# Kernel tuning notes

Measured on AMD Instinct MI355X. Metric: run time of the kernel, lower is better.

## Reference

```python
import jax, jax.numpy as jnp
import numpy as np
from jax import lax

# fixed body-part graph: column j lists source nodes i with adj[i,j]!=0
PART_LIST_LIST = [[1], [0, 2, 3, 4], [1], [1], [1, 5], [4]]
HID = 10
IN_DIM = 256


def conv1x1(x, W):  # x:[B,C,H,W], W:[O,C]
    return jnp.einsum('bchw,oc->bohw', x, W)


def bn(x, s, t):  # eval-mode BN folded to per-channel affine
    return x * s[None, :, None, None] + t[None, :, None, None]


def relation(x, W1, s1, t1, W2, s2, t2):
    h = jax.nn.relu(bn(conv1x1(x, W1), s1, t1))
    return jax.nn.relu(bn(conv1x1(h, W2), s2, t2))


def conv3x3(x, W, b):
    y = lax.conv_general_dilated(x, W, (1, 1), 'SAME',
                                 dimension_numbers=('NCHW', 'OIHW', 'NCHW'))
    return y + b[None, :, None, None]


def gru_step(msg, h, Wg, bg, Wc, bc):
    # one ConvGRU step: gates from cat([input, h]), candidate from cat([input, r*h])
    gates = jax.nn.sigmoid(conv3x3(jnp.concatenate([msg, h], axis=1), Wg, bg))
    r, u = jnp.split(gates, 2, axis=1)
    cand = jnp.tanh(conv3x3(jnp.concatenate([msg, r * h], axis=1), Wc, bc))
    return (1.0 - u) * h + u * cand


def _forward(f_node, h_nodes, p_nodes, xp,
             W_dau, b_dau, W_dal, b_dal,
             W_dec1, dec1_s, dec1_t, W_dec2, dec2_s, dec2_t,
             W_att0, W_att1, W_att2, W_att3, W_att4, W_att5, b_att,
             W_proj, proj_s, proj_t, Wg, bg, Wc, bc):
    # decomposition attention maps (Decomp_att): 1x1 conv with bias
    decomp_map_u = conv1x1(h_nodes[0], W_dau) + b_dau[None, :, None, None]  # [B,5,H,W]
    decomp_map_l = conv1x1(h_nodes[1], W_dal) + b_dal[None, :, None, None]  # [B,3,H,W]
    att_u = jax.nn.softmax(decomp_map_u, axis=1)
    att_l = jax.nn.softmax(decomp_map_l, axis=1)

    # Decomposition: relation(cat([parent*att_{i+1}, child_i])), shared weights
    def decomp(parent, child, a):
        return relation(jnp.concatenate([parent * a, child], axis=1),
                        W_dec1, dec1_s, dec1_t, W_dec2, dec2_s, dec2_t)

    dec_u = [decomp(h_nodes[0], p_nodes[i], att_u[:, i + 1:i + 2]) for i in range(4)]
    dec_l = [decomp(h_nodes[1], p_nodes[4 + i], att_l[:, i + 1:i + 2]) for i in range(2)]
    decomp_msgs = jnp.stack(dec_u + dec_l)  # [6,B,10,H,W]

    # Contexture: per-node attention over concatenated neighbor features
    W_atts = [W_att0, W_att1, W_att2, W_att3, W_att4, W_att5]
    atts = []
    for i, plist in enumerate(PART_LIST_LIST):
        ctx = jnp.concatenate([p_nodes[j] for j in plist], axis=1)
        atts.append(jax.nn.sigmoid(conv1x1(ctx, W_atts[i]) + b_att[i]))
    Fdep_att = jnp.stack(atts)  # [6,B,1,H,W]

    modulated = xp[None] * (2.0 - Fdep_att)                     # [6,B,256,H,W]
    proj = jnp.einsum('nbchw,noc->nbohw', modulated, W_proj)    # [6,B,10,H,W]
    proj = jax.nn.relu(proj * proj_s[:, None, :, None, None]
                       + proj_t[:, None, :, None, None])

    message = decomp_msgs + proj
    # per-node ConvGRU update (hidden state = p_node)
    xp_new = jax.vmap(gru_step)(message, p_nodes, Wg, bg, Wc, bc)  # [6,B,10,H,W]
    return xp_new, decomp_map_u, decomp_map_l, Fdep_att


def setup_inputs() -> dict:
    key = jax.random.key(0)
    ks = jax.random.split(key, 32)
    B, H, W = 4, 128, 128
    hd, cd = HID, IN_DIM

    def rn(k, shape, s=0.05):
        return jax.random.normal(k, shape, jnp.float32) * s

    inp = {}
    inp['f_node'] = rn(ks[0], (B, hd, H, W), 1.0)
    inp['h_nodes'] = rn(ks[1], (2, B, hd, H, W), 1.0)
    inp['p_nodes'] = rn(ks[2], (6, B, hd, H, W), 1.0)
    inp['xp'] = rn(ks[3], (B, cd, H, W), 1.0)
    inp['W_dau'] = rn(ks[4], (5, hd));  inp['b_dau'] = rn(ks[5], (5,))
    inp['W_dal'] = rn(ks[6], (3, hd));  inp['b_dal'] = rn(ks[7], (3,))
    inp['W_dec1'] = rn(ks[8], (2 * hd, 2 * hd))
    inp['dec1_s'] = 1.0 + rn(ks[9], (2 * hd,)); inp['dec1_t'] = rn(ks[10], (2 * hd,))
    inp['W_dec2'] = rn(ks[11], (hd, 2 * hd))
    inp['dec2_s'] = 1.0 + rn(ks[12], (hd,));    inp['dec2_t'] = rn(ks[13], (hd,))
    lens = [len(p) for p in PART_LIST_LIST]  # [1,4,1,1,2,1]
    for i in range(6):
        inp[f'W_att{i}'] = rn(ks[14 + i], (1, hd * lens[i]))
    inp['b_att'] = rn(ks[20], (6,))
    inp['W_proj'] = rn(ks[21], (6, hd, cd))
    inp['proj_s'] = 1.0 + rn(ks[22], (6, hd)); inp['proj_t'] = rn(ks[23], (6, hd))
    inp['Wg'] = rn(ks[24], (6, 2 * hd, 2 * hd, 3, 3)); inp['bg'] = rn(ks[25], (6, 2 * hd))
    inp['Wc'] = rn(ks[26], (6, hd, 2 * hd, 3, 3));     inp['bc'] = rn(ks[27], (6, hd))
    return inp


def reference(f_node, h_nodes, p_nodes, xp,
              W_dau, b_dau, W_dal, b_dal,
              W_dec1, dec1_s, dec1_t, W_dec2, dec2_s, dec2_t,
              W_att0, W_att1, W_att2, W_att3, W_att4, W_att5, b_att,
              W_proj, proj_s, proj_t, Wg, bg, Wc, bc):
    return _forward(f_node, h_nodes, p_nodes, xp,
                    W_dau, b_dau, W_dal, b_dal,
                    W_dec1, dec1_s, dec1_t, W_dec2, dec2_s, dec2_t,
                    W_att0, W_att1, W_att2, W_att3, W_att4, W_att5, b_att,
                    W_proj, proj_s, proj_t, Wg, bg, Wc, bc)
```

## Files before the change

### kernel.cpp

```cpp
#include <hip/hip_runtime.h>
#include <math.h>

#define HW    16384
#define WID   128
#define NB    4
#define OFF_U 3932160
#define OFF_L 4259840
#define OFF_F 4456448

#define TCH   24
#define TROW  132
#define T6_N  (6*TROW*TCH)
#define WG_ELEMS   (9*32*TCH)
#define WC_ELEMS   (9*16*TCH)

typedef __attribute__((ext_vector_type(8))) short  short8_t;
typedef __attribute__((ext_vector_type(4))) float  float4_t;

__device__ __forceinline__ float sig_(float x)  { return 1.f/(1.f+__expf(-x)); }
__device__ __forceinline__ float tanh_(float x) { float e=__expf(2.f*x); return 1.f - 2.f/(e+1.f); }
__device__ __forceinline__ unsigned pk2bf(float a, float b){
  unsigned r;
  asm("v_cvt_pk_bf16_f32 %0, %1, %2" : "=v"(r) : "v"(a), "v"(b));
  return r;
}
__device__ __forceinline__ float bf2f(unsigned short s){
  return __uint_as_float(((unsigned)s) << 16);
}
__device__ __forceinline__ int swz1536(int bi){ return (bi & 7)*192 + (bi >> 3); }
__device__ __forceinline__ int swz768 (int bi){ return (bi & 7)*96  + (bi >> 3); }

__global__ __launch_bounds__(256)
void k_att_dec(const float* __restrict__ hn, const float* __restrict__ pnn,
               const float* __restrict__ Wdau, const float* __restrict__ bdau,
               const float* __restrict__ Wdal, const float* __restrict__ bdal,
               const float* __restrict__ Wd1, const float* __restrict__ s1v, const float* __restrict__ t1v,
               const float* __restrict__ Wd2, const float* __restrict__ s2v, const float* __restrict__ t2v,
               const float* __restrict__ Wa0, const float* __restrict__ Wa1, const float* __restrict__ Wa2,
               const float* __restrict__ Wa3, const float* __restrict__ Wa4, const float* __restrict__ Wa5,
               const float* __restrict__ batt,
               float* __restrict__ out, unsigned* __restrict__ wmsg_p)
{
  const int bi  = swz1536(blockIdx.x);
  const int n   = bi >> 8;
  const int g   = (bi & 255)*256 + threadIdx.x;
  const int b   = g >> 14;
  const int pix = g & 16383;

  float h[10];
  float a;
  if (n < 4){
#pragma unroll
    for (int c=0;c<10;c++) h[c] = hn[(b*10+c)*HW + pix];
    float v[5]; float mx = -1e30f;
#pragma unroll
    for (int o=0;o<5;o++){
      float t = bdau[o];
#pragma unroll
      for (int c=0;c<10;c++) t += Wdau[o*10+c]*h[c];
      if (n==0) out[OFF_U + (b*5+o)*HW + pix] = t;
      v[o]=t; mx = fmaxf(mx,t);
    }
    float s=0.f;
#pragma unroll
    for (int o=0;o<5;o++){ v[o]=__expf(v[o]-mx); s+=v[o]; }
    a = v[n+1]/s;
  } else {
#pragma unroll
    for (int c=0;c<10;c++) h[c] = hn[((NB+b)*10+c)*HW + pix];
    float v[3]; float mx = -1e30f;
#pragma unroll
    for (int o=0;o<3;o++){
      float t = bdal[o];
#pragma unroll
      for (int c=0;c<10;c++) t += Wdal[o*10+c]*h[c];
      if (n==4) out[OFF_L + (b*3+o)*HW + pix] = t;
      v[o]=t; mx = fmaxf(mx,t);
    }
    float s=0.f;
#pragma unroll
    for (int o=0;o<3;o++){ v[o]=__expf(v[o]-mx); s+=v[o]; }
    a = v[n-3]/s;
  }

  float child[10];
#pragma unroll
  for (int c=0;c<10;c++) child[c] = pnn[((n*NB+b)*10+c)*HW + pix];

  float af = batt[n];
  if (n==0){
#pragma unroll
    for (int c=0;c<10;c++) af += Wa0[c]*pnn[((1*NB+b)*10+c)*HW+pix];
  } else if (n==1){
#pragma unroll
    for (int c=0;c<10;c++){
      af += Wa1[c]   *pnn[((0*NB+b)*10+c)*HW+pix];
      af += Wa1[10+c]*pnn[((2*NB+b)*10+c)*HW+pix];
      af += Wa1[20+c]*pnn[((3*NB+b)*10+c)*HW+pix];
      af += Wa1[30+c]*pnn[((4*NB+b)*10+c)*HW+pix];
    }
  } else if (n==2){
#pragma unroll
    for (int c=0;c<10;c++) af += Wa2[c]*pnn[((1*NB+b)*10+c)*HW+pix];
  } else if (n==3){
#pragma unroll
    for (int c=0;c<10;c++) af += Wa3[c]*pnn[((1*NB+b)*10+c)*HW+pix];
  } else if (n==4){
#pragma unroll
    for (int c=0;c<10;c++){
      af += Wa4[c]   *pnn[((1*NB+b)*10+c)*HW+pix];
      af += Wa4[10+c]*pnn[((5*NB+b)*10+c)*HW+pix];
    }
  } else {
#pragma unroll
    for (int c=0;c<10;c++) af += Wa5[c]*pnn[((4*NB+b)*10+c)*HW+pix];
  }
  out[OFF_F + (n*NB+b)*HW + pix] = sig_(af);

  float x20[20];
#pragma unroll
  for (int c=0;c<10;c++){ x20[c]=h[c]*a; x20[10+c]=child[c]; }
  float h20[20];
#pragma unroll
  for (int o=0;o<20;o++){
    float acc=0.f;
#pragma unroll
    for (int c=0;c<20;c++) acc += Wd1[o*20+c]*x20[c];
    h20[o] = fmaxf(acc*s1v[o]+t1v[o], 0.f);
  }
  float msg10[10];
#pragma unroll
  for (int o=0;o<10;o++){
    float acc=0.f;
#pragma unroll
    for (int c=0;c<20;c++) acc += Wd2[o*20+c]*h20[c];
    msg10[o] = fmaxf(acc*s2v[o]+t2v[o], 0.f);
  }
#pragma unroll
  for (int p=0;p<5;p++)
    wmsg_p[((size_t)((n*NB+b)*5 + p))*HW + pix] = pk2bf(msg10[2*p], msg10[2*p+1]);
}

__global__ __launch_bounds__(256, 2)
void k_proj(const float* __restrict__ xp, const float* __restrict__ Wp,
            const float* __restrict__ ps, const float* __restrict__ pt,
            const float* __restrict__ outf, unsigned* __restrict__ wmsg_p)
{
  __shared__ __align__(16) unsigned short wlds[64*264];
  const int tid = threadIdx.x;

#pragma unroll
  for (int it=0; it<16; ++it){
    const int e = tid + it*256;
    const int row = e >> 6, q = e & 63;
    uint2 pk; pk.x = 0u; pk.y = 0u;
    if (row < 60){
      const float s = ps[row];
      float4 wv = *reinterpret_cast<const float4*>(Wp + row*256 + q*4);
      pk.x = pk2bf(wv.x*s, wv.y*s);
      pk.y = pk2bf(wv.z*s, wv.w*s);
    }
    *reinterpret_cast<uint2*>(&wlds[row*264 + q*4]) = pk;
  }
  __syncthreads();

  const int l  = tid & 63;
  const int w  = tid >> 6;
  const int lr = l & 15;
  const int lk = l >> 4;

  const int tile = blockIdx.x*4 + w;
  const int P    = tile*16;
  const int b    = P >> 14;
  const int pixb = P & 16383;
  const int px   = pixb + lr;

  const float* xb = xp + (size_t)(b*256)*HW + px;
  float v[64];
#pragma unroll
  for (int ks=0; ks<8; ++ks)
#pragma unroll
    for (int j=0; j<8; ++j)
      v[ks*8+j] = xb[(size_t)(ks*32 + lk*8 + j)*HW];

  short8_t bf[8];
#pragma unroll
  for (int ks=0; ks<8; ++ks){
    union { short8_t s; unsigned u[4]; } bu;
#pragma unroll
    for (int jp=0; jp<4; ++jp)
      bu.u[jp] = pk2bf(v[ks*8+2*jp], v[ks*8+2*jp+1]);
    bf[ks] = bu.s;
  }

  float4_t acc[4];
#pragma unroll
  for (int nf=0;nf<4;nf++){ acc[nf][0]=0.f; acc[nf][1]=0.f; acc[nf][2]=0.f; acc[nf][3]=0.f; }

#pragma unroll
  for (int ks=0; ks<8; ++ks){
#pragma unroll
    for (int nf=0; nf<4; ++nf){
      short8_t wa = *reinterpret_cast<const short8_t*>(&wlds[(nf*16+lr)*264 + ks*32 + lk*8]);
      acc[nf] = __builtin_amdgcn_mfma_f32_16x16x32_bf16(wa, bf[ks], acc[nf], 0,0,0);
    }
  }

#pragma unroll
  for (int nf=0;nf<4;nf++){
#pragma unroll
    for (int jp=0;jp<2;jp++){
      const int row0 = nf*16 + lk*4 + 2*jp;
      if (row0 < 60){
        const unsigned nn = (unsigned)row0 / 10u;
        const int o = row0 - (int)nn*10;
        float att = outf[OFF_F + (nn*NB+b)*HW + pixb + lr];
        float f   = 2.f - att;
        float v0 = fmaxf(f*acc[nf][2*jp]   + pt[row0],   0.f);
        float v1 = fmaxf(f*acc[nf][2*jp+1] + pt[row0+1], 0.f);
        size_t idx = ((size_t)((nn*NB+b)*5 + (o>>1)))*HW + pixb + lr;
        unsigned old = wmsg_p[idx];
        float d0 = bf2f((unsigned short)(old & 0xffffu)) + v0;
        float d1 = bf2f((unsigned short)(old >> 16))     + v1;
        wmsg_p[idx] = pk2bf(d0, d1);
      }
    }
  }
}

__global__ __launch_bounds__(256, 3)
void k_gru_gates(const float* __restrict__ pnn, const float* __restrict__ Wg,
                 const float* __restrict__ bg,
                 const unsigned* __restrict__ wmsg_p, unsigned* __restrict__ wrh_p,
                 unsigned* __restrict__ wu_p)
{
  __shared__ __align__(16) unsigned short tl[T6_N];
  __shared__ __align__(16) unsigned short wl[WG_ELEMS];
  const int bi = swz768(blockIdx.x);
  const int n  = bi >> 7;
  const int b  = (bi >> 5) & 3;
  const int y0 = (bi & 31) * 4;
  const int tid = threadIdx.x;

  const int base_nb  = (n*NB+b)*10;
  const int base_nb5 = (n*NB+b)*5;
  const float* pb = pnn + (size_t)base_nb*HW;

  short8_t zz = {0,0,0,0,0,0,0,0};
#pragma unroll
  for (int it=0; it<10; ++it){
    const int e = tid*8 + it*2048;
    if (e < T6_N) *reinterpret_cast<short8_t*>(&tl[e]) = zz;
  }
#pragma unroll
  for (int it=0; it<4; ++it){
    const int e = tid*8 + it*2048;
    if (e < WG_ELEMS) *reinterpret_cast<short8_t*>(&wl[e]) = zz;
  }
  __syncthreads();

  const float* Wn = Wg + n*3600;
#pragma unroll
  for (int it=0; it<8; ++it){
    const int e = tid + it*256;
    if (e < 1800){
      int sh = e/200, rem = e - sh*200, o = rem/10, chp = rem - o*10;
      float w0 = Wn[o*180 + (2*chp  )*9 + sh];
      float w1 = Wn[o*180 + (2*chp+1)*9 + sh];
      *reinterpret_cast<unsigned*>(&wl[(sh*32+o)*TCH + 2*chp]) = pk2bf(w0, w1);
    }
  }
#pragma unroll
  for (int it=0; it<30; ++it){
    const int e = tid + it*256;
    int row = e/1280, rem = e - row*1280, chp = rem>>7, x = rem&127;
    int yy = y0 - 1 + row;
    if ((unsigned)yy < 128u){
      unsigned pk;
      if (chp < 5){
        pk = wmsg_p[((size_t)(base_nb5 + chp))*HW + yy*WID + x];
      } else {
        const float* s0 = pb + (size_t)(2*chp-10)*HW;
        pk = pk2bf(s0[yy*WID + x], s0[HW + yy*WID + x]);
      }
      *reinterpret_cast<unsigned*>(&tl[(row*TROW + x+1)*TCH + 2*chp]) = pk;
    }
  }
  __syncthreads();

  const int l  = tid & 63;
  const int w  = tid >> 6;
  const int lr = l & 15;
  const int lk = l >> 4;

  short8_t wa0[9], wa1[9];
#pragma unroll
  for (int sh=0; sh<9; sh++){
    wa0[sh] = (lk<3) ? *reinterpret_cast<const short8_t*>(&wl[(sh*32 +      lr)*TCH + lk*8]) : zz;
    wa1[sh] = (lk<3) ? *reinterpret_cast<const short8_t*>(&wl[(sh*32 + 16 + lr)*TCH + lk*8]) : zz;
  }
  float bs0[4], bs1[4];
#pragma unroll
  for (int j=0;j<4;j++){
    int o = lk*4 + j;
    bs0[j] = bg[n*20 + o];
    int o1 = 16 + lk*4 + j;
    bs1[j] = (o1 < 20) ? bg[n*20 + o1] : 0.f;
  }

  for (int t=0; t<8; ++t){
    const int tile  = w*8 + t;
    const int row_t = tile >> 3;
    const int xloc  = (tile & 7) * 16;

    float4_t a0 = {0.f,0.f,0.f,0.f}, a1 = {0.f,0.f,0.f,0.f};
#pragma unroll
    for (int sh=0; sh<9; sh++){
      const int dy = sh/3, dx = sh - dy*3;
      const int addr = ((row_t + dy)*TROW + (xloc + lr + dx))*TCH + lk*8;
      short8_t bf = (lk<3) ? *reinterpret_cast<const short8_t*>(&tl[addr]) : zz;
      a0 = __builtin_amdgcn_mfma_f32_16x16x32_bf16(wa0[sh], bf, a0, 0,0,0);
      a1 = __builtin_amdgcn_mfma_f32_16x16x32_bf16(wa1[sh], bf, a1, 0,0,0);
    }

    const int pix = (y0 + row_t)*WID + xloc + lr;
#pragma unroll
    for (int jp=0; jp<2; ++jp){
      const int j0 = 2*jp;
      const int o  = lk*4 + j0;
      float g0 = sig_(a0[j0]   + bs0[j0]);
      float g1 = sig_(a0[j0+1] + bs0[j0+1]);
      if (o < 10){
        float h0 = pb[(size_t)o*HW + pix];
        float h1 = pb[(size_t)(o+1)*HW + pix];
        wrh_p[((size_t)(base_nb5 + (o>>1)))*HW + pix] = pk2bf(g0*h0, g1*h1);
      } else {
        wu_p[((size_t)(base_nb5 + ((o-10)>>1)))*HW + pix] = pk2bf(g0, g1);
      }
    }
    if (lk == 0){
#pragma unroll
      for (int jp=0; jp<2; ++jp){
        const int j0 = 2*jp;
        const int o1 = 16 + j0;
        float g0 = sig_(a1[j0]   + bs1[j0]);
        float g1 = sig_(a1[j0+1] + bs1[j0+1]);
        wu_p[((size_t)(base_nb5 + ((o1-10)>>1)))*HW + pix] = pk2bf(g0, g1);
      }
    }
  }
}

__global__ __launch_bounds__(256, 3)
void k_gru_out(const float* __restrict__ pnn, const float* __restrict__ Wc,
               const float* __restrict__ bc,
               const unsigned* __restrict__ wmsg_p, const unsigned* __restrict__ wrh_p,
               const unsigned* __restrict__ wu_p, float* __restrict__ out)
{
  __shared__ __align__(16) unsigned short tl[T6_N];
  __shared__ __align__(16) unsigned short wl[WC_ELEMS];
  const int bi = swz768(blockIdx.x);
  const int n  = bi >> 7;
  const int b  = (bi >> 5) & 3;
  const int y0 = (bi & 31) * 4;
  const int tid = threadIdx.x;

  const int base_nb  = (n*NB+b)*10;
  const int base_nb5 = (n*NB+b)*5;
  const float* pb = pnn + (size_t)base_nb*HW;

  short8_t zz = {0,0,0,0,0,0,0,0};
#pragma unroll
  for (int it=0; it<10; ++it){
    const int e = tid*8 + it*2048;
    if (e < T6_N) *reinterpret_cast<short8_t*>(&tl[e]) = zz;
  }
#pragma unroll
  for (int it=0; it<2; ++it){
    const int e = tid*8 + it*2048;
    if (e < WC_ELEMS) *reinterpret_cast<short8_t*>(&wl[e]) = zz;
  }
  __syncthreads();

  const float* Wn = Wc + n*1800;
#pragma unroll
  for (int it=0; it<4; ++it){
    const int e = tid + it*256;
    if (e < 900){
      int sh = e/100, rem = e - sh*100, o = rem/10, chp = rem - o*10;
      float w0 = Wn[o*180 + (2*chp  )*9 + sh];
      float w1 = Wn[o*180 + (2*chp+1)*9 + sh];
      *reinterpret_cast<unsigned*>(&wl[(sh*16+o)*TCH + 2*chp]) = pk2bf(w0, w1);
    }
  }
#pragma unroll
  for (int it=0; it<30; ++it){
    const int e = tid + it*256;
    int row = e/1280, rem = e - row*1280, chp = rem>>7, x = rem&127;
    int yy = y0 - 1 + row;
    if ((unsigned)yy < 128u){
      unsigned pk;
      if (chp < 5){
        pk = wmsg_p[((size_t)(base_nb5 + chp))*HW + yy*WID + x];
      } else {
        pk = wrh_p[((size_t)(base_nb5 + (chp-5)))*HW + yy*WID + x];
      }
      *reinterpret_cast<unsigned*>(&tl[(row*TROW + x+1)*TCH + 2*chp]) = pk;
    }
  }
  __syncthreads();

  const int l  = tid & 63;
  const int w  = tid >> 6;
  const int lr = l & 15;
  const int lk = l >> 4;

  short8_t wa[9];
#pragma unroll
  for (int sh=0; sh<9; sh++)
    wa[sh] = (lk<3) ? *reinterpret_cast<const short8_t*>(&wl[(sh*16 + lr)*TCH + lk*8]) : zz;

  float bs[4];
#pragma unroll
  for (int j=0;j<4;j++){
    int o = lk*4 + j;
    bs[j] = (o < 10) ? bc[n*10 + o] : 0.f;
  }

  for (int t=0; t<8; ++t){
    const int tile  = w*8 + t;
    const int row_t = tile >> 3;
    const int xloc  = (tile & 7) * 16;

    float4_t a0 = {0.f,0.f,0.f,0.f};
#pragma unroll
    for (int sh=0; sh<9; sh++){
      const int dy = sh/3, dx = sh - dy*3;
      const int addr = ((row_t + dy)*TROW + (xloc + lr + dx))*TCH + lk*8;
      short8_t bf = (lk<3) ? *reinterpret_cast<const short8_t*>(&tl[addr]) : zz;
      a0 = __builtin_amdgcn_mfma_f32_16x16x32_bf16(wa[sh], bf, a0, 0,0,0);
    }

    const int pix = (y0 + row_t)*WID + xloc + lr;
#pragma unroll
    for (int jp=0; jp<2; ++jp){
      const int j0 = 2*jp;
      const int o  = lk*4 + j0;
      if (o < 10){
        unsigned up = wu_p[((size_t)(base_nb5 + (o>>1)))*HW + pix];
        float u0 = bf2f((unsigned short)(up & 0xffffu));
        float u1 = bf2f((unsigned short)(up >> 16));
        float h0 = pb[(size_t)o*HW + pix];
        float h1 = pb[(size_t)(o+1)*HW + pix];
        float c0 = tanh_(a0[j0]   + bs[j0]);
        float c1 = tanh_(a0[j0+1] + bs[j0+1]);
        out[(size_t)(base_nb+o  )*HW + pix] = (1.f-u0)*h0 + u0*c0;
        out[(size_t)(base_nb+o+1)*HW + pix] = (1.f-u1)*h1 + u1*c1;
      }
    }
  }
}

extern "C" void kernel_launch(void* const* d_in, const int* in_sizes, int n_in,
                              void* d_out, int out_size, void* d_ws, size_t ws_size,
                              hipStream_t stream)
{
  (void)in_sizes; (void)n_in; (void)out_size; (void)ws_size;
  const float* hn   = (const float*)d_in[1];
  const float* pnn  = (const float*)d_in[2];
  const float* xp   = (const float*)d_in[3];
  const float* Wdau = (const float*)d_in[4];
  const float* bdau = (const float*)d_in[5];
  const float* Wdal = (const float*)d_in[6];
  const float* bdal = (const float*)d_in[7];
  const float* Wd1  = (const float*)d_in[8];
  const float* s1v  = (const float*)d_in[9];
  const float* t1v  = (const float*)d_in[10];
  const float* Wd2  = (const float*)d_in[11];
  const float* s2v  = (const float*)d_in[12];
  const float* t2v  = (const float*)d_in[13];
  const float* Wa0  = (const float*)d_in[14];
  const float* Wa1  = (const float*)d_in[15];
  const float* Wa2  = (const float*)d_in[16];
  const float* Wa3  = (const float*)d_in[17];
  const float* Wa4  = (const float*)d_in[18];
  const float* Wa5  = (const float*)d_in[19];
  const float* batt = (const float*)d_in[20];
  const float* Wp   = (const float*)d_in[21];
  const float* ps   = (const float*)d_in[22];
  const float* pt   = (const float*)d_in[23];
  const float* Wg   = (const float*)d_in[24];
  const float* bg   = (const float*)d_in[25];
  const float* Wc   = (const float*)d_in[26];
  const float* bc   = (const float*)d_in[27];

  float* out = (float*)d_out;
  float* wsf = (float*)d_ws;
  unsigned* ws_msg = (unsigned*)wsf;
  unsigned* ws_rh  = (unsigned*)(wsf + 1966080);
  unsigned* ws_u   = (unsigned*)(wsf + 3932160);

  k_att_dec<<<dim3(1536), dim3(256), 0, stream>>>(hn, pnn, Wdau, bdau, Wdal, bdal,
      Wd1, s1v, t1v, Wd2, s2v, t2v, Wa0, Wa1, Wa2, Wa3, Wa4, Wa5, batt, out, ws_msg);
  k_proj<<<dim3(1024), dim3(256), 0, stream>>>(xp, Wp, ps, pt, (const float*)d_out, ws_msg);
  k_gru_gates<<<dim3(768), dim3(256), 0, stream>>>(pnn, Wg, bg, ws_msg, ws_rh, ws_u);
  k_gru_out<<<dim3(768), dim3(256), 0, stream>>>(pnn, Wc, bc, ws_msg, ws_rh, ws_u, out);
}
```

Before: 88.59 us.

## Compute decomposition relation MLP with bf16 MFMA via LDS staging

Replaces the per-thread scalar fp32 20x20 and 10x20 1x1-conv MLP in k_att_dec with bf16 MFMA 16x16x32 tiles. Inputs and hidden activations are staged through shared memory, and the BN scale is folded into bf16 weights. This cuts VALU FMA work at the cost of LDS traffic, extra barriers, zero-init and reduced precision in the hidden layer. The kernel is likely memory-bound, so the gain may be small.

After: 85.27 us. 1.04x faster.

```diff
diff --git a/kernel.cpp b/kernel.cpp
--- a/kernel.cpp
+++ b/kernel.cpp
@@ -41,11 +41,40 @@
                const float* __restrict__ batt,
                float* __restrict__ out, unsigned* __restrict__ wmsg_p)
 {
-  const int bi  = swz1536(blockIdx.x);
-  const int n   = bi >> 8;
-  const int g   = (bi & 255)*256 + threadIdx.x;
-  const int b   = g >> 14;
-  const int pix = g & 16383;
+  __shared__ __align__(16) unsigned short xl [256*TCH];
+  __shared__ __align__(16) unsigned short hl [256*TCH];
+  __shared__ __align__(16) unsigned short wl1[32*TCH];
+  __shared__ __align__(16) unsigned short wl2[16*TCH];
+
+  const int bi    = swz1536(blockIdx.x);
+  const int n     = bi >> 8;
+  const int chunk = bi & 255;
+  const int b     = chunk >> 6;
+  const int pixbase = (chunk & 63) * 256;
+  const int tid   = threadIdx.x;
+  const int pix   = pixbase + tid;
+
+  short8_t zz = {0,0,0,0,0,0,0,0};
+#pragma unroll
+  for (int it=0; it<3; ++it) *reinterpret_cast<short8_t*>(&xl[tid*8 + it*2048]) = zz;
+#pragma unroll
+  for (int it=0; it<3; ++it) *reinterpret_cast<short8_t*>(&hl[tid*8 + it*2048]) = zz;
+  if (tid < 96)  *reinterpret_cast<short8_t*>(&wl1[tid*8]) = zz;
+  if (tid < 48)  *reinterpret_cast<short8_t*>(&wl2[tid*8]) = zz;
+  __syncthreads();
+
+  if (tid < 200){
+    int o = tid/10, chp = tid - o*10;
+    float s = s1v[o];
+    *reinterpret_cast<unsigned*>(&wl1[o*TCH + 2*chp]) =
+        pk2bf(Wd1[o*20 + 2*chp]*s, Wd1[o*20 + 2*chp+1]*s);
+  } else if (tid < 300){
+    int e = tid - 200;
+    int o = e/10, chp = e - o*10;
+    float s = s2v[o];
+    *reinterpret_cast<unsigned*>(&wl2[o*TCH + 2*chp]) =
+        pk2bf(Wd2[o*20 + 2*chp]*s, Wd2[o*20 + 2*chp+1]*s);
+  }
 
   float h[10];
   float a;
@@ -117,28 +146,79 @@
   }
   out[OFF_F + (n*NB+b)*HW + pix] = sig_(af);
 
-  float x20[20];
-#pragma unroll
-  for (int c=0;c<10;c++){ x20[c]=h[c]*a; x20[10+c]=child[c]; }
-  float h20[20];
-#pragma unroll
-  for (int o=0;o<20;o++){
-    float acc=0.f;
-#pragma unroll
-    for (int c=0;c<20;c++) acc += Wd1[o*20+c]*x20[c];
-    h20[o] = fmaxf(acc*s1v[o]+t1v[o], 0.f);
-  }
-  float msg10[10];
-#pragma unroll
-  for (int o=0;o<10;o++){
-    float acc=0.f;
-#pragma unroll
-    for (int c=0;c<20;c++) acc += Wd2[o*20+c]*h20[c];
-    msg10[o] = fmaxf(acc*s2v[o]+t2v[o], 0.f);
-  }
 #pragma unroll
   for (int p=0;p<5;p++)
-    wmsg_p[((size_t)((n*NB+b)*5 + p))*HW + pix] = pk2bf(msg10[2*p], msg10[2*p+1]);
+    *reinterpret_cast<unsigned*>(&xl[tid*TCH + 2*p])    = pk2bf(h[2*p]*a, h[2*p+1]*a);
+#pragma unroll
+  for (int p=0;p<5;p++)
+    *reinterpret_cast<unsigned*>(&xl[tid*TCH + 10 + 2*p]) = pk2bf(child[2*p], child[2*p+1]);
+  __syncthreads();
+
+  const int l  = tid & 63;
+  const int w  = tid >> 6;
+  const int lr = l & 15;
+  const int lk = l >> 4;
+
+  short8_t wa0 = (lk<3) ? *reinterpret_cast<const short8_t*>(&wl1[lr*TCH      + lk*8]) : zz;
+  short8_t wa1 = (lk<3) ? *reinterpret_cast<const short8_t*>(&wl1[(16+lr)*TCH + lk*8]) : zz;
+  float t1a[4], t1b[4];
+#pragma unroll
+  for (int j=0;j<4;j++){
+    t1a[j] = t1v[lk*4 + j];
+    int o1 = 16 + lk*4 + j;
+    t1b[j] = (o1 < 20) ? t1v[o1] : 0.f;
+  }
+
+#pragma unroll
+  for (int t=0; t<4; ++t){
+    const int tile = w*4 + t;
+    short8_t bf = (lk<3) ? *reinterpret_cast<const short8_t*>(&xl[(tile*16+lr)*TCH + lk*8]) : zz;
+    float4_t a0 = {0.f,0.f,0.f,0.f}, a1 = {0.f,0.f,0.f,0.f};
+    a0 = __builtin_amdgcn_mfma_f32_16x16x32_bf16(wa0, bf, a0, 0,0,0);
+    a1 = __builtin_amdgcn_mfma_f32_16x16x32_bf16(wa1, bf, a1, 0,0,0);
+    const int rowb = (tile*16+lr)*TCH;
+#pragma unroll
+    for (int jp=0; jp<2; ++jp){
+      float v0 = fmaxf(a0[2*jp]   + t1a[2*jp],   0.f);
+      float v1 = fmaxf(a0[2*jp+1] + t1a[2*jp+1], 0.f);
+      *reinterpret_cast<unsigned*>(&hl[rowb + lk*4 + 2*jp]) = pk2bf(v0, v1);
+    }
+    if (lk == 0){
+#pragma unroll
+      for (int jp=0; jp<2; ++jp){
+        float v0 = fmaxf(a1[2*jp]   + t1b[2*jp],   0.f);
+        float v1 = fmaxf(a1[2*jp+1] + t1b[2*jp+1], 0.f);
+        *reinterpret_cast<unsigned*>(&hl[rowb + 16 + 2*jp]) = pk2bf(v0, v1);
+      }
+    }
+  }
+  __syncthreads();
+
+  short8_t wa2 = (lk<3) ? *reinterpret_cast<const short8_t*>(&wl2[lr*TCH + lk*8]) : zz;
+  float t2a[4];
+#pragma unroll
+  for (int j=0;j<4;j++){
+    int o = lk*4 + j;
+    t2a[j] = (o < 10) ? t2v[o] : 0.f;
+  }
+
+#pragma unroll
+  for (int t=0; t<4; ++t){
+    const int tile = w*4 + t;
+    short8_t bf = (lk<3) ? *reinterpret_cast<const short8_t*>(&hl[(tile*16+lr)*TCH + lk*8]) : zz;
+    float4_t c = {0.f,0.f,0.f,0.f};
+    c = __builtin_amdgcn_mfma_f32_16x16x32_bf16(wa2, bf, c, 0,0,0);
+    const int pixT = pixbase + tile*16 + lr;
+#pragma unroll
+    for (int jp=0; jp<2; ++jp){
+      const int o0 = lk*4 + 2*jp;
+      if (o0 < 10){
+        float v0 = fmaxf(c[2*jp]   + t2a[2*jp],   0.f);
+        float v1 = fmaxf(c[2*jp+1] + t2a[2*jp+1], 0.f);
+        wmsg_p[((size_t)((n*NB+b)*5 + (o0>>1)))*HW + pixT] = pk2bf(v0, v1);
+      }
+    }
+  }
 }
 
 __global__ __launch_bounds__(256, 2)
```
